# Kernel tuning notes

Hardware: AMD Instinct MI355X
Metric: run time of the kernel (lower is better)

Reference implementation:

```python
import jax, jax.numpy as jnp
import numpy as np

B, N, H, W, D = 4, 8, 32, 32, 64

def setup_inputs() -> dict:
    key = jax.random.key(0)
    k1, k2, k3, k4 = jax.random.split(key, 4)
    scale = D ** (-0.5)
    q = jax.random.normal(k1, (B, N, H, W, D), dtype=jnp.float32)
    k = jax.random.normal(k2, (B, N, H, W, D), dtype=jnp.float32)
    # learned absolute position embeddings, init N(mean=scale, std=1) per nn.init.normal_(t, scale)
    ph = jax.random.normal(k3, (H, D), dtype=jnp.float32) + scale
    pw = jax.random.normal(k4, (W, D), dtype=jnp.float32) + scale
    return {"q": q, "k": k, "ph": ph, "pw": pw}

def reference(q, k, ph, pw):
    # content-content logits: [b,n,H,W,H,W]
    logits = jnp.einsum('bnhwd,bnpqd->bnhwpq', q, k)
    # absolute positional bias: emb[p,q,d] = ph[p,d] + pw[q,d]
    emb = ph[:, None, :] + pw[None, :, :]            # [H, W, D]
    logits = logits + jnp.einsum('bnxyd,pqd->bnxypq', q, emb)
    return logits
```

## Files before the change

kernel.cpp:

```cpp
#include <hip/hip_runtime.h>


typedef __bf16 bf16x8 __attribute__((ext_vector_type(8)));
typedef __bf16 bf16x4 __attribute__((ext_vector_type(4)));
typedef float  f32x16 __attribute__((ext_vector_type(16)));

#define LDSTRIDE 72

__global__ __launch_bounds__(512)
void abs_pos_emb_gemm(const float* __restrict__ q,
                      const float* __restrict__ k,
                      const float* __restrict__ ph,
                      const float* __restrict__ pw,
                      float* __restrict__ out)
{
    extern __shared__ __bf16 lds[];
    __bf16* As = lds;
    __bf16* Bs = lds + 256 * LDSTRIDE;

    const int tid = threadIdx.x;
    const int bid = blockIdx.x;
    const int batch = ((bid & 7) << 2) + (bid >> 7);
    const int tile  = (bid >> 3) & 15;
    const int trow  = (tile >> 2) << 8;
    const int tcol  = (tile & 3)  << 8;

    const float* Qb = q + (size_t)batch * (1024 * 64);
    const float* Kb = k + (size_t)batch * (1024 * 64);

#pragma unroll
    for (int i = 0; i < 8; ++i) {
        int f   = i * 512 + tid;
        int row = f >> 4;
        int col = (f & 15) << 2;
        float4 v = *reinterpret_cast<const float4*>(
            Qb + (size_t)(trow + row) * 64 + col);
        bf16x4 h;
        h[0] = (__bf16)v.x; h[1] = (__bf16)v.y;
        h[2] = (__bf16)v.z; h[3] = (__bf16)v.w;
        *reinterpret_cast<bf16x4*>(&As[row * LDSTRIDE + col]) = h;
    }

#pragma unroll
    for (int i = 0; i < 8; ++i) {
        int f   = i * 512 + tid;
        int row = f >> 4;
        int col = (f & 15) << 2;
        int grow = tcol + row;
        int p  = grow >> 5;
        int qq = grow & 31;
        float4 v  = *reinterpret_cast<const float4*>(
            Kb + (size_t)grow * 64 + col);
        float4 vp = *reinterpret_cast<const float4*>(ph + p  * 64 + col);
        float4 vw = *reinterpret_cast<const float4*>(pw + qq * 64 + col);
        bf16x4 h;
        h[0] = (__bf16)(v.x + vp.x + vw.x);
        h[1] = (__bf16)(v.y + vp.y + vw.y);
        h[2] = (__bf16)(v.z + vp.z + vw.z);
        h[3] = (__bf16)(v.w + vp.w + vw.w);
        *reinterpret_cast<bf16x4*>(&Bs[row * LDSTRIDE + col]) = h;
    }

    __syncthreads();

    const int lane = tid & 63;
    const int wid  = tid >> 6;
    const int wr   = (wid >> 1) << 6;
    const int wc   = (wid & 1)  << 7;
    const int fr   = lane & 31;
    const int fk   = (lane >> 5) << 3;

    f32x16 acc[2][4] = {};

#pragma unroll
    for (int kk = 0; kk < 4; ++kk) {
        const int kb = kk * 16 + fk;
        bf16x8 a0 = *reinterpret_cast<const bf16x8*>(&As[(wr      + fr) * LDSTRIDE + kb]);
        bf16x8 a1 = *reinterpret_cast<const bf16x8*>(&As[(wr + 32 + fr) * LDSTRIDE + kb]);
        bf16x8 b0 = *reinterpret_cast<const bf16x8*>(&Bs[(wc       + fr) * LDSTRIDE + kb]);
        bf16x8 b1 = *reinterpret_cast<const bf16x8*>(&Bs[(wc +  32 + fr) * LDSTRIDE + kb]);
        bf16x8 b2 = *reinterpret_cast<const bf16x8*>(&Bs[(wc +  64 + fr) * LDSTRIDE + kb]);
        bf16x8 b3 = *reinterpret_cast<const bf16x8*>(&Bs[(wc +  96 + fr) * LDSTRIDE + kb]);
        acc[0][0] = __builtin_amdgcn_mfma_f32_32x32x16_bf16(a0, b0, acc[0][0], 0, 0, 0);
        acc[0][1] = __builtin_amdgcn_mfma_f32_32x32x16_bf16(a0, b1, acc[0][1], 0, 0, 0);
        acc[0][2] = __builtin_amdgcn_mfma_f32_32x32x16_bf16(a0, b2, acc[0][2], 0, 0, 0);
        acc[0][3] = __builtin_amdgcn_mfma_f32_32x32x16_bf16(a0, b3, acc[0][3], 0, 0, 0);
        acc[1][0] = __builtin_amdgcn_mfma_f32_32x32x16_bf16(a1, b0, acc[1][0], 0, 0, 0);
        acc[1][1] = __builtin_amdgcn_mfma_f32_32x32x16_bf16(a1, b1, acc[1][1], 0, 0, 0);
        acc[1][2] = __builtin_amdgcn_mfma_f32_32x32x16_bf16(a1, b2, acc[1][2], 0, 0, 0);
        acc[1][3] = __builtin_amdgcn_mfma_f32_32x32x16_bf16(a1, b3, acc[1][3], 0, 0, 0);
    }

    float* Ob = out + (size_t)batch * (1024u * 1024u);
    const int srow = trow + wr + ((lane >> 5) << 2);
    const int scol = tcol + wc + (lane & 31);

#pragma unroll
    for (int m = 0; m < 2; ++m) {
#pragma unroll
        for (int r = 0; r < 16; ++r) {
            int roff = (r & 3) + ((r >> 2) << 3);
            float* po = Ob + (size_t)(srow + m * 32 + roff) * 1024 + scol;
#pragma unroll
            for (int n = 0; n < 4; ++n) {
                po[n * 32] = acc[m][n][r];
            }
        }
    }
}

extern "C" void kernel_launch(void* const* d_in, const int* in_sizes, int n_in,
                              void* d_out, int out_size, void* d_ws, size_t ws_size,
                              hipStream_t stream) {
    const float* q  = (const float*)d_in[0];
    const float* k  = (const float*)d_in[1];
    const float* ph = (const float*)d_in[2];
    const float* pw = (const float*)d_in[3];
    float* out = (float*)d_out;

    size_t lds_bytes = 2u * 256u * LDSTRIDE * sizeof(__bf16);
    hipLaunchKernelGGL(abs_pos_emb_gemm, dim3(512), dim3(512), lds_bytes, stream,
                       q, k, ph, pw, out);
}
```

Baseline: 30.95 us.

## Compute two output column tiles per block, reusing Q tile and prefetching K

Halves the grid from 512 to 256 blocks so each block computes two adjacent 256x256 output tiles. The Q tile in LDS is reused for both, and the second K tile's global loads are issued before the first tile's stores, overlapping them. The aim is to cut redundant Q loads and per-block launch overhead. In exchange it uses more LDS and registers and exposes less parallelism, since 256 blocks is roughly one wave per CU on a 256-CU part.

```diff
diff --git a/kernel.cpp b/kernel.cpp
--- a/kernel.cpp
+++ b/kernel.cpp
@@ -15,18 +15,21 @@
                       float* __restrict__ out)
 {
     extern __shared__ __bf16 lds[];
-    __bf16* As = lds;
-    __bf16* Bs = lds + 256 * LDSTRIDE;
+    __bf16* As  = lds;
+    __bf16* Bs0 = lds + 256 * LDSTRIDE;
+    __bf16* Bs1 = lds + 512 * LDSTRIDE;
 
     const int tid = threadIdx.x;
     const int bid = blockIdx.x;
-    const int batch = ((bid & 7) << 2) + (bid >> 7);
-    const int tile  = (bid >> 3) & 15;
-    const int trow  = (tile >> 2) << 8;
-    const int tcol  = (tile & 3)  << 8;
+    const int batch = ((bid & 7) << 2) + (bid >> 6);
+    const int j     = (bid >> 3) & 7;
+    const int trow  = (j >> 1) << 8;
+    const int tcol0 = (j & 1) << 9;
+    const int tcol1 = tcol0 + 256;
 
     const float* Qb = q + (size_t)batch * (1024 * 64);
     const float* Kb = k + (size_t)batch * (1024 * 64);
+    float* Ob = out + (size_t)batch * (1024u * 1024u);
 
 #pragma unroll
     for (int i = 0; i < 8; ++i) {
@@ -46,7 +49,7 @@
         int f   = i * 512 + tid;
         int row = f >> 4;
         int col = (f & 15) << 2;
-        int grow = tcol + row;
+        int grow = tcol0 + row;
         int p  = grow >> 5;
         int qq = grow & 31;
         float4 v  = *reinterpret_cast<const float4*>(
@@ -58,7 +61,7 @@
         h[1] = (__bf16)(v.y + vp.y + vw.y);
         h[2] = (__bf16)(v.z + vp.z + vw.z);
         h[3] = (__bf16)(v.w + vp.w + vw.w);
-        *reinterpret_cast<bf16x4*>(&Bs[row * LDSTRIDE + col]) = h;
+        *reinterpret_cast<bf16x4*>(&Bs0[row * LDSTRIDE + col]) = h;
     }
 
     __syncthreads();
@@ -70,17 +73,23 @@
     const int fr   = lane & 31;
     const int fk   = (lane >> 5) << 3;
 
-    f32x16 acc[2][4] = {};
+    f32x16 acc[2][4];
+#pragma unroll
+    for (int m = 0; m < 2; ++m)
+#pragma unroll
+        for (int n2 = 0; n2 < 4; ++n2)
+#pragma unroll
+            for (int e = 0; e < 16; ++e) acc[m][n2][e] = 0.0f;
 
 #pragma unroll
     for (int kk = 0; kk < 4; ++kk) {
         const int kb = kk * 16 + fk;
         bf16x8 a0 = *reinterpret_cast<const bf16x8*>(&As[(wr      + fr) * LDSTRIDE + kb]);
         bf16x8 a1 = *reinterpret_cast<const bf16x8*>(&As[(wr + 32 + fr) * LDSTRIDE + kb]);
-        bf16x8 b0 = *reinterpret_cast<const bf16x8*>(&Bs[(wc       + fr) * LDSTRIDE + kb]);
-        bf16x8 b1 = *reinterpret_cast<const bf16x8*>(&Bs[(wc +  32 + fr) * LDSTRIDE + kb]);
-        bf16x8 b2 = *reinterpret_cast<const bf16x8*>(&Bs[(wc +  64 + fr) * LDSTRIDE + kb]);
-        bf16x8 b3 = *reinterpret_cast<const bf16x8*>(&Bs[(wc +  96 + fr) * LDSTRIDE + kb]);
+        bf16x8 b0 = *reinterpret_cast<const bf16x8*>(&Bs0[(wc      + fr) * LDSTRIDE + kb]);
+        bf16x8 b1 = *reinterpret_cast<const bf16x8*>(&Bs0[(wc + 32 + fr) * LDSTRIDE + kb]);
+        bf16x8 b2 = *reinterpret_cast<const bf16x8*>(&Bs0[(wc + 64 + fr) * LDSTRIDE + kb]);
+        bf16x8 b3 = *reinterpret_cast<const bf16x8*>(&Bs0[(wc + 96 + fr) * LDSTRIDE + kb]);
         acc[0][0] = __builtin_amdgcn_mfma_f32_32x32x16_bf16(a0, b0, acc[0][0], 0, 0, 0);
         acc[0][1] = __builtin_amdgcn_mfma_f32_32x32x16_bf16(a0, b1, acc[0][1], 0, 0, 0);
         acc[0][2] = __builtin_amdgcn_mfma_f32_32x32x16_bf16(a0, b2, acc[0][2], 0, 0, 0);
@@ -91,19 +100,91 @@
         acc[1][3] = __builtin_amdgcn_mfma_f32_32x32x16_bf16(a1, b3, acc[1][3], 0, 0, 0);
     }
 
-    float* Ob = out + (size_t)batch * (1024u * 1024u);
+    float4 kv[8];
+#pragma unroll
+    for (int i = 0; i < 8; ++i) {
+        int f   = i * 512 + tid;
+        int row = f >> 4;
+        int col = (f & 15) << 2;
+        kv[i] = *reinterpret_cast<const float4*>(
+            Kb + (size_t)(tcol1 + row) * 64 + col);
+    }
+
     const int srow = trow + wr + ((lane >> 5) << 2);
-    const int scol = tcol + wc + (lane & 31);
-
-#pragma unroll
-    for (int m = 0; m < 2; ++m) {
-#pragma unroll
-        for (int r = 0; r < 16; ++r) {
-            int roff = (r & 3) + ((r >> 2) << 3);
-            float* po = Ob + (size_t)(srow + m * 32 + roff) * 1024 + scol;
-#pragma unroll
-            for (int n = 0; n < 4; ++n) {
-                po[n * 32] = acc[m][n][r];
+    {
+        const int scol = tcol0 + wc + (lane & 31);
+#pragma unroll
+        for (int m = 0; m < 2; ++m) {
+#pragma unroll
+            for (int r = 0; r < 16; ++r) {
+                int roff = (r & 3) + ((r >> 2) << 3);
+                float* po = Ob + (size_t)(srow + m * 32 + roff) * 1024 + scol;
+#pragma unroll
+                for (int n2 = 0; n2 < 4; ++n2) {
+                    po[n2 * 32] = acc[m][n2][r];
+                }
+            }
+        }
+    }
+
+#pragma unroll
+    for (int i = 0; i < 8; ++i) {
+        int f   = i * 512 + tid;
+        int row = f >> 4;
+        int col = (f & 15) << 2;
+        int grow = tcol1 + row;
+        int p  = grow >> 5;
+        int qq = grow & 31;
+        float4 vp = *reinterpret_cast<const float4*>(ph + p  * 64 + col);
+        float4 vw = *reinterpret_cast<const float4*>(pw + qq * 64 + col);
+        bf16x4 h;
+        h[0] = (__bf16)(kv[i].x + vp.x + vw.x);
+        h[1] = (__bf16)(kv[i].y + vp.y + vw.y);
+        h[2] = (__bf16)(kv[i].z + vp.z + vw.z);
+        h[3] = (__bf16)(kv[i].w + vp.w + vw.w);
+        *reinterpret_cast<bf16x4*>(&Bs1[row * LDSTRIDE + col]) = h;
+    }
+
+    __syncthreads();
+
+#pragma unroll
+    for (int m = 0; m < 2; ++m)
+#pragma unroll
+        for (int n2 = 0; n2 < 4; ++n2)
+#pragma unroll
+            for (int e = 0; e < 16; ++e) acc[m][n2][e] = 0.0f;
+
+#pragma unroll
+    for (int kk = 0; kk < 4; ++kk) {
+        const int kb = kk * 16 + fk;
+        bf16x8 a0 = *reinterpret_cast<const bf16x8*>(&As[(wr      + fr) * LDSTRIDE + kb]);
+        bf16x8 a1 = *reinterpret_cast<const bf16x8*>(&As[(wr + 32 + fr) * LDSTRIDE + kb]);
+        bf16x8 b0 = *reinterpret_cast<const bf16x8*>(&Bs1[(wc      + fr) * LDSTRIDE + kb]);
+        bf16x8 b1 = *reinterpret_cast<const bf16x8*>(&Bs1[(wc + 32 + fr) * LDSTRIDE + kb]);
+        bf16x8 b2 = *reinterpret_cast<const bf16x8*>(&Bs1[(wc + 64 + fr) * LDSTRIDE + kb]);
+        bf16x8 b3 = *reinterpret_cast<const bf16x8*>(&Bs1[(wc + 96 + fr) * LDSTRIDE + kb]);
+        acc[0][0] = __builtin_amdgcn_mfma_f32_32x32x16_bf16(a0, b0, acc[0][0], 0, 0, 0);
+        acc[0][1] = __builtin_amdgcn_mfma_f32_32x32x16_bf16(a0, b1, acc[0][1], 0, 0, 0);
+        acc[0][2] = __builtin_amdgcn_mfma_f32_32x32x16_bf16(a0, b2, acc[0][2], 0, 0, 0);
+        acc[0][3] = __builtin_amdgcn_mfma_f32_32x32x16_bf16(a0, b3, acc[0][3], 0, 0, 0);
+        acc[1][0] = __builtin_amdgcn_mfma_f32_32x32x16_bf16(a1, b0, acc[1][0], 0, 0, 0);
+        acc[1][1] = __builtin_amdgcn_mfma_f32_32x32x16_bf16(a1, b1, acc[1][1], 0, 0, 0);
+        acc[1][2] = __builtin_amdgcn_mfma_f32_32x32x16_bf16(a1, b2, acc[1][2], 0, 0, 0);
+        acc[1][3] = __builtin_amdgcn_mfma_f32_32x32x16_bf16(a1, b3, acc[1][3], 0, 0, 0);
+    }
+
+    {
+        const int scol = tcol1 + wc + (lane & 31);
+#pragma unroll
+        for (int m = 0; m < 2; ++m) {
+#pragma unroll
+            for (int r = 0; r < 16; ++r) {
+                int roff = (r & 3) + ((r >> 2) << 3);
+                float* po = Ob + (size_t)(srow + m * 32 + roff) * 1024 + scol;
+#pragma unroll
+                for (int n2 = 0; n2 < 4; ++n2) {
+                    po[n2 * 32] = acc[m][n2][r];
+                }
             }
         }
     }
@@ -118,7 +199,7 @@
     const float* pw = (const float*)d_in[3];
     float* out = (float*)d_out;
 
-    size_t lds_bytes = 2u * 256u * LDSTRIDE * sizeof(__bf16);
-    hipLaunchKernelGGL(abs_pos_emb_gemm, dim3(512), dim3(512), lds_bytes, stream,
+    size_t lds_bytes = 3u * 256u * LDSTRIDE * sizeof(__bf16);
+    hipLaunchKernelGGL(abs_pos_emb_gemm, dim3(256), dim3(512), lds_bytes, stream,
                        q, k, ph, pw, out);
 }
```

Measured after the change: 29.94 us. 3.3% less time.

## Stream B tiles through double-buffered LDS and interleave stores with MFMA

Applied to the files above, without the earlier changes.

Each block now covers a 256x512 output region with 256 blocks instead of 512 blocks of 256x256. It walks 8 column chunks of 64, double-buffering the K+pos-embedding tile in LDS and prefetching the next chunk's global loads while the current chunk computes and stores. The aim is to overlap output stores, which dominate this write-bound kernel, with loading and compute, and to cut accumulator register pressure. The cost is fewer blocks (less parallelism across CUs), a barrier per chunk, and smaller MFMA work per chunk.

```diff
diff --git a/kernel.cpp b/kernel.cpp
--- a/kernel.cpp
+++ b/kernel.cpp
@@ -15,18 +15,20 @@
                       float* __restrict__ out)
 {
     extern __shared__ __bf16 lds[];
-    __bf16* As = lds;
-    __bf16* Bs = lds + 256 * LDSTRIDE;
+    __bf16* As  = lds;
+    __bf16* Bs0 = lds + 256 * LDSTRIDE;
+    __bf16* Bs1 = lds + 320 * LDSTRIDE;
 
     const int tid = threadIdx.x;
     const int bid = blockIdx.x;
-    const int batch = ((bid & 7) << 2) + (bid >> 7);
-    const int tile  = (bid >> 3) & 15;
-    const int trow  = (tile >> 2) << 8;
-    const int tcol  = (tile & 3)  << 8;
+    const int batch = ((bid & 7) << 2) + (bid >> 6);
+    const int j     = (bid >> 3) & 7;
+    const int trow  = (j >> 1) << 8;
+    const int tcol0 = (j & 1) << 9;
 
     const float* Qb = q + (size_t)batch * (1024 * 64);
     const float* Kb = k + (size_t)batch * (1024 * 64);
+    float* Ob = out + (size_t)batch * (1024u * 1024u);
 
 #pragma unroll
     for (int i = 0; i < 8; ++i) {
@@ -42,15 +44,14 @@
     }
 
 #pragma unroll
-    for (int i = 0; i < 8; ++i) {
+    for (int i = 0; i < 2; ++i) {
         int f   = i * 512 + tid;
         int row = f >> 4;
         int col = (f & 15) << 2;
-        int grow = tcol + row;
+        int grow = tcol0 + row;
         int p  = grow >> 5;
         int qq = grow & 31;
-        float4 v  = *reinterpret_cast<const float4*>(
-            Kb + (size_t)grow * 64 + col);
+        float4 v  = *reinterpret_cast<const float4*>(Kb + (size_t)grow * 64 + col);
         float4 vp = *reinterpret_cast<const float4*>(ph + p  * 64 + col);
         float4 vw = *reinterpret_cast<const float4*>(pw + qq * 64 + col);
         bf16x4 h;
@@ -58,53 +59,79 @@
         h[1] = (__bf16)(v.y + vp.y + vw.y);
         h[2] = (__bf16)(v.z + vp.z + vw.z);
         h[3] = (__bf16)(v.w + vp.w + vw.w);
-        *reinterpret_cast<bf16x4*>(&Bs[row * LDSTRIDE + col]) = h;
+        *reinterpret_cast<bf16x4*>(&Bs0[row * LDSTRIDE + col]) = h;
     }
 
     __syncthreads();
 
     const int lane = tid & 63;
     const int wid  = tid >> 6;
-    const int wr   = (wid >> 1) << 6;
-    const int wc   = (wid & 1)  << 7;
+    const int wrow = (wid >> 1) << 6;
+    const int wcl  = (wid & 1)  << 5;
     const int fr   = lane & 31;
     const int fk   = (lane >> 5) << 3;
+    const int srow = trow + wrow + ((lane >> 5) << 2);
 
-    f32x16 acc[2][4] = {};
+    const int prow0 = tid >> 4;
+    const int prow1 = prow0 + 32;
+    const int pcol  = (tid & 15) << 2;
 
 #pragma unroll
-    for (int kk = 0; kk < 4; ++kk) {
-        const int kb = kk * 16 + fk;
-        bf16x8 a0 = *reinterpret_cast<const bf16x8*>(&As[(wr      + fr) * LDSTRIDE + kb]);
-        bf16x8 a1 = *reinterpret_cast<const bf16x8*>(&As[(wr + 32 + fr) * LDSTRIDE + kb]);
-        bf16x8 b0 = *reinterpret_cast<const bf16x8*>(&Bs[(wc       + fr) * LDSTRIDE + kb]);
-        bf16x8 b1 = *reinterpret_cast<const bf16x8*>(&Bs[(wc +  32 + fr) * LDSTRIDE + kb]);
-        bf16x8 b2 = *reinterpret_cast<const bf16x8*>(&Bs[(wc +  64 + fr) * LDSTRIDE + kb]);
-        bf16x8 b3 = *reinterpret_cast<const bf16x8*>(&Bs[(wc +  96 + fr) * LDSTRIDE + kb]);
-        acc[0][0] = __builtin_amdgcn_mfma_f32_32x32x16_bf16(a0, b0, acc[0][0], 0, 0, 0);
-        acc[0][1] = __builtin_amdgcn_mfma_f32_32x32x16_bf16(a0, b1, acc[0][1], 0, 0, 0);
-        acc[0][2] = __builtin_amdgcn_mfma_f32_32x32x16_bf16(a0, b2, acc[0][2], 0, 0, 0);
-        acc[0][3] = __builtin_amdgcn_mfma_f32_32x32x16_bf16(a0, b3, acc[0][3], 0, 0, 0);
-        acc[1][0] = __builtin_amdgcn_mfma_f32_32x32x16_bf16(a1, b0, acc[1][0], 0, 0, 0);
-        acc[1][1] = __builtin_amdgcn_mfma_f32_32x32x16_bf16(a1, b1, acc[1][1], 0, 0, 0);
-        acc[1][2] = __builtin_amdgcn_mfma_f32_32x32x16_bf16(a1, b2, acc[1][2], 0, 0, 0);
-        acc[1][3] = __builtin_amdgcn_mfma_f32_32x32x16_bf16(a1, b3, acc[1][3], 0, 0, 0);
-    }
+    for (int c = 0; c < 8; ++c) {
+        const __bf16* B  = (c & 1) ? Bs1 : Bs0;
+        __bf16*       Bn = (c & 1) ? Bs0 : Bs1;
 
-    float* Ob = out + (size_t)batch * (1024u * 1024u);
-    const int srow = trow + wr + ((lane >> 5) << 2);
-    const int scol = tcol + wc + (lane & 31);
+        float4 kv0, kv1, vp0, vp1, vw0, vw1;
+        if (c < 7) {
+            int g0 = tcol0 + (c + 1) * 64 + prow0;
+            int g1 = tcol0 + (c + 1) * 64 + prow1;
+            kv0 = *reinterpret_cast<const float4*>(Kb + (size_t)g0 * 64 + pcol);
+            kv1 = *reinterpret_cast<const float4*>(Kb + (size_t)g1 * 64 + pcol);
+            vp0 = *reinterpret_cast<const float4*>(ph + (g0 >> 5) * 64 + pcol);
+            vp1 = *reinterpret_cast<const float4*>(ph + (g1 >> 5) * 64 + pcol);
+            vw0 = *reinterpret_cast<const float4*>(pw + (g0 & 31) * 64 + pcol);
+            vw1 = *reinterpret_cast<const float4*>(pw + (g1 & 31) * 64 + pcol);
+        }
 
+        f32x16 acc0 = {};
+        f32x16 acc1 = {};
 #pragma unroll
-    for (int m = 0; m < 2; ++m) {
+        for (int kk = 0; kk < 4; ++kk) {
+            const int kb = kk * 16 + fk;
+            bf16x8 a0 = *reinterpret_cast<const bf16x8*>(&As[(wrow      + fr) * LDSTRIDE + kb]);
+            bf16x8 a1 = *reinterpret_cast<const bf16x8*>(&As[(wrow + 32 + fr) * LDSTRIDE + kb]);
+            bf16x8 b0 = *reinterpret_cast<const bf16x8*>(&B [(wcl       + fr) * LDSTRIDE + kb]);
+            acc0 = __builtin_amdgcn_mfma_f32_32x32x16_bf16(a0, b0, acc0, 0, 0, 0);
+            acc1 = __builtin_amdgcn_mfma_f32_32x32x16_bf16(a1, b0, acc1, 0, 0, 0);
+        }
+
+        {
+            const int scol = tcol0 + (c << 6) + wcl + fr;
 #pragma unroll
-        for (int r = 0; r < 16; ++r) {
-            int roff = (r & 3) + ((r >> 2) << 3);
-            float* po = Ob + (size_t)(srow + m * 32 + roff) * 1024 + scol;
+            for (int r = 0; r < 16; ++r) {
+                int roff = (r & 3) + ((r >> 2) << 3);
+                Ob[(size_t)(srow + roff) * 1024 + scol]      = acc0[r];
+            }
 #pragma unroll
-            for (int n = 0; n < 4; ++n) {
-                po[n * 32] = acc[m][n][r];
+            for (int r = 0; r < 16; ++r) {
+                int roff = (r & 3) + ((r >> 2) << 3);
+                Ob[(size_t)(srow + 32 + roff) * 1024 + scol] = acc1[r];
             }
+        }
+
+        if (c < 7) {
+            bf16x4 h0, h1;
+            h0[0] = (__bf16)(kv0.x + vp0.x + vw0.x);
+            h0[1] = (__bf16)(kv0.y + vp0.y + vw0.y);
+            h0[2] = (__bf16)(kv0.z + vp0.z + vw0.z);
+            h0[3] = (__bf16)(kv0.w + vp0.w + vw0.w);
+            h1[0] = (__bf16)(kv1.x + vp1.x + vw1.x);
+            h1[1] = (__bf16)(kv1.y + vp1.y + vw1.y);
+            h1[2] = (__bf16)(kv1.z + vp1.z + vw1.z);
+            h1[3] = (__bf16)(kv1.w + vp1.w + vw1.w);
+            *reinterpret_cast<bf16x4*>(&Bn[prow0 * LDSTRIDE + pcol]) = h0;
+            *reinterpret_cast<bf16x4*>(&Bn[prow1 * LDSTRIDE + pcol]) = h1;
+            __syncthreads();
         }
     }
 }
@@ -118,7 +145,7 @@
     const float* pw = (const float*)d_in[3];
     float* out = (float*)d_out;
 
-    size_t lds_bytes = 2u * 256u * LDSTRIDE * sizeof(__bf16);
-    hipLaunchKernelGGL(abs_pos_emb_gemm, dim3(512), dim3(512), lds_bytes, stream,
+    size_t lds_bytes = (256u + 128u) * LDSTRIDE * sizeof(__bf16);
+    hipLaunchKernelGGL(abs_pos_emb_gemm, dim3(256), dim3(512), lds_bytes, stream,
                        q, k, ph, pw, out);
 }
```

After: 28.68 us (median of 2 runs). 1.08x faster.
